# Kernel tuning notes

Hardware: AMD Instinct MI355X
Metric: run time of the kernel (lower is better)

Reference implementation:

```python
import jax, jax.numpy as jnp
import numpy as np

NUM_ZONES = 256  # number of distinct zone ids per image (fill_max of zones)


def setup_inputs() -> dict:
    key = jax.random.key(0)
    k1, k2 = jax.random.split(key)
    B, H, W = 64, 512, 512
    inp = jax.random.normal(k1, (B, 1, H, W), dtype=jnp.float32)
    zones = jax.random.randint(k2, (B, H, W), 0, NUM_ZONES, dtype=jnp.int32)
    return {"input": inp, "zones": zones}


def reference(input, zones):
    # zones branch of CenterExtractor.forward: per-batch scatter_max over zone ids.
    # For each batch element, keep the pixel holding the maximum heatmap value
    # within each zone (segmented argmax), producing a boolean center mask.
    B = input.shape[0]
    x = input.reshape(B, -1)   # [B, N] flattened heatmap
    z = zones.reshape(B, -1)   # [B, N] segment ids

    # per-batch segmented max: [B, NUM_ZONES]
    seg_max = jax.vmap(
        lambda xv, zv: jax.ops.segment_max(xv, zv, num_segments=NUM_ZONES)
    )(x, z)

    # pixel is a center iff it attains its zone's max (ties measure-zero for randn;
    # empty zones have seg_max = -inf and match nothing, mirroring idxs != N filter)
    mask = x == jnp.take_along_axis(seg_max, z, axis=1)  # [B, N] bool

    centermask = mask.reshape(input.shape)  # [B, 1, H, W] bool
    n_centers = jnp.sum(centermask)
    return centermask, n_centers
```

## Files before the change

kernel.cpp:

```cpp
#include <hip/hip_runtime.h>

#define NZ   256
#define NB   64
#define NPIX (512 * 512)

__device__ __forceinline__ unsigned enc(float f) {
    unsigned b = __float_as_uint(f);
    return b ^ ((b & 0x80000000u) ? 0xFFFFFFFFu : 0x80000000u);
}
__device__ __forceinline__ float dec(unsigned u) {
    unsigned b = (u & 0x80000000u) ? (u ^ 0x80000000u) : ~u;
    return __uint_as_float(b);
}

__global__ __launch_bounds__(256) void segmax_kernel(
        const float* __restrict__ inp, const int* __restrict__ zones,
        unsigned* __restrict__ segmax) {
    __shared__ unsigned smax[NZ];
    const int t = threadIdx.x;
    smax[t] = 0u;
    __syncthreads();

    const int blocksPerBatch = NPIX / (256 * 16);
    const int batch = blockIdx.x / blocksPerBatch;
    const int chunk = blockIdx.x % blocksPerBatch;
    const long base = (long)batch * NPIX + (long)chunk * (256 * 16);
    const float4* in4 = (const float4*)(inp + base);
    const int4*   z4  = (const int4*)(zones + base);

#pragma unroll
    for (int it = 0; it < 4; ++it) {
        float4 v = in4[it * 256 + t];
        int4   z = z4[it * 256 + t];
        atomicMax(&smax[z.x], enc(v.x));
        atomicMax(&smax[z.y], enc(v.y));
        atomicMax(&smax[z.z], enc(v.z));
        atomicMax(&smax[z.w], enc(v.w));
    }
    __syncthreads();

    unsigned m = smax[t];
    if (m) atomicMax(&segmax[batch * NZ + t], m);
}

__global__ __launch_bounds__(256) void mask_kernel(
        const float* __restrict__ inp, const int* __restrict__ zones,
        const unsigned* __restrict__ segmax,
        int* __restrict__ mask, int* __restrict__ partial) {
    __shared__ float smax[NZ];
    __shared__ int wsum[4];
    const int t = threadIdx.x;

    const int blocksPerBatch = NPIX / (256 * 16);
    const int batch = blockIdx.x / blocksPerBatch;
    const int chunk = blockIdx.x % blocksPerBatch;

    smax[t] = dec(segmax[batch * NZ + t]);
    __syncthreads();

    const long base = (long)batch * NPIX + (long)chunk * (256 * 16);
    const float4* in4 = (const float4*)(inp + base);
    const int4*   z4  = (const int4*)(zones + base);
    int4* m4 = (int4*)(mask + base);

    int c = 0;
#pragma unroll
    for (int it = 0; it < 4; ++it) {
        float4 v = in4[it * 256 + t];
        int4   z = z4[it * 256 + t];
        int4 m;
        m.x = (v.x == smax[z.x]) ? 1 : 0;
        m.y = (v.y == smax[z.y]) ? 1 : 0;
        m.z = (v.z == smax[z.z]) ? 1 : 0;
        m.w = (v.w == smax[z.w]) ? 1 : 0;
        m4[it * 256 + t] = m;
        c += m.x + m.y + m.z + m.w;
    }

#pragma unroll
    for (int off = 32; off; off >>= 1) c += __shfl_down(c, off);
    if ((t & 63) == 0) wsum[t >> 6] = c;
    __syncthreads();
    if (t == 0) partial[blockIdx.x] = wsum[0] + wsum[1] + wsum[2] + wsum[3];
}

__global__ __launch_bounds__(256) void count_kernel(
        const int* __restrict__ partial, int n, int* __restrict__ count) {
    __shared__ int wsum[4];
    const int t = threadIdx.x;
    int c = 0;
    for (int i = t; i < n; i += 256) c += partial[i];
#pragma unroll
    for (int off = 32; off; off >>= 1) c += __shfl_down(c, off);
    if ((t & 63) == 0) wsum[t >> 6] = c;
    __syncthreads();
    if (t == 0) *count = wsum[0] + wsum[1] + wsum[2] + wsum[3];
}

extern "C" void kernel_launch(void* const* d_in, const int* in_sizes, int n_in,
                              void* d_out, int out_size, void* d_ws, size_t ws_size,
                              hipStream_t stream) {
    const float* inp   = (const float*)d_in[0];
    const int*   zones = (const int*)d_in[1];
    int*         out   = (int*)d_out;
    unsigned*    segmx = (unsigned*)d_ws;
    int*         partial = (int*)((char*)d_ws + NB * NZ * sizeof(unsigned));

    const long nmask = (long)NB * NPIX;
    const int nblocks = NB * (NPIX / 4096);

    hipMemsetAsync(d_ws, 0, (size_t)NB * NZ * sizeof(unsigned), stream);

    segmax_kernel<<<nblocks, 256, 0, stream>>>(inp, zones, segmx);
    mask_kernel<<<nblocks, 256, 0, stream>>>(inp, zones, segmx, out, partial);
    count_kernel<<<1, 256, 0, stream>>>(partial, nblocks, out + nmask);
}
```

Before: 59.23 us.

## Replace global atomics with per-block partial maxima and a separate reduce kernel

The segmented-max stage now writes each block's shared-memory maxima to a partials buffer instead of doing global atomicMax. A new reduce kernel combines the partials per batch and decodes them to floats, which also removes the memset. Each block now processes 32 elements per thread, with all loads batched ahead of the LDS atomics behind a sched_barrier to overlap memory latency. The cost is an extra kernel launch and a round trip of the partials through global memory.

```diff
diff --git a/kernel.cpp b/kernel.cpp
--- a/kernel.cpp
+++ b/kernel.cpp
@@ -1,8 +1,17 @@
 #include <hip/hip_runtime.h>
 
-#define NZ   256
-#define NB   64
-#define NPIX (512 * 512)
+#define NZ    256
+#define NB    64
+#define NPIX  (512 * 512)
+
+#define EPT1  32
+#define CHUNK1 (256 * EPT1)
+#define BPB1  (NPIX / CHUNK1)
+#define NBLK1 (NB * BPB1)
+
+#define CHUNK3 (256 * 16)
+#define BPB3  (NPIX / CHUNK3)
+#define NBLK3 (NB * BPB3)
 
 __device__ __forceinline__ unsigned enc(float f) {
     unsigned b = __float_as_uint(f);
@@ -13,52 +22,69 @@
     return __uint_as_float(b);
 }
 
-__global__ __launch_bounds__(256) void segmax_kernel(
+__global__ __launch_bounds__(256) void segmax_part(
         const float* __restrict__ inp, const int* __restrict__ zones,
-        unsigned* __restrict__ segmax) {
+        unsigned* __restrict__ part) {
     __shared__ unsigned smax[NZ];
     const int t = threadIdx.x;
     smax[t] = 0u;
     __syncthreads();
 
-    const int blocksPerBatch = NPIX / (256 * 16);
-    const int batch = blockIdx.x / blocksPerBatch;
-    const int chunk = blockIdx.x % blocksPerBatch;
-    const long base = (long)batch * NPIX + (long)chunk * (256 * 16);
+    const int batch = blockIdx.x / BPB1;
+    const int chunk = blockIdx.x % BPB1;
+    const long base = (long)batch * NPIX + (long)chunk * CHUNK1;
     const float4* in4 = (const float4*)(inp + base);
     const int4*   z4  = (const int4*)(zones + base);
 
 #pragma unroll
-    for (int it = 0; it < 4; ++it) {
-        float4 v = in4[it * 256 + t];
-        int4   z = z4[it * 256 + t];
-        atomicMax(&smax[z.x], enc(v.x));
-        atomicMax(&smax[z.y], enc(v.y));
-        atomicMax(&smax[z.z], enc(v.z));
-        atomicMax(&smax[z.w], enc(v.w));
+    for (int h = 0; h < EPT1 / 16; ++h) {
+        float4 v[4];
+        int4   z[4];
+#pragma unroll
+        for (int i = 0; i < 4; ++i) {
+            const int idx = (h * 4 + i) * 256 + t;
+            v[i] = in4[idx];
+            z[i] = z4[idx];
+        }
+        __builtin_amdgcn_sched_barrier(0);
+#pragma unroll
+        for (int i = 0; i < 4; ++i) {
+            atomicMax(&smax[z[i].x], enc(v[i].x));
+            atomicMax(&smax[z[i].y], enc(v[i].y));
+            atomicMax(&smax[z[i].z], enc(v[i].z));
+            atomicMax(&smax[z[i].w], enc(v[i].w));
+        }
     }
     __syncthreads();
+    part[(long)blockIdx.x * NZ + t] = smax[t];
+}
 
-    unsigned m = smax[t];
-    if (m) atomicMax(&segmax[batch * NZ + t], m);
+__global__ __launch_bounds__(256) void segmax_reduce(
+        const unsigned* __restrict__ part, float* __restrict__ segf) {
+    const int t = threadIdx.x;
+    const int batch = blockIdx.x;
+    const unsigned* p = part + (long)batch * BPB1 * NZ;
+    unsigned m = 0u;
+#pragma unroll 8
+    for (int c = 0; c < BPB1; ++c) m = max(m, p[c * NZ + t]);
+    segf[batch * NZ + t] = dec(m);
 }
 
 __global__ __launch_bounds__(256) void mask_kernel(
         const float* __restrict__ inp, const int* __restrict__ zones,
-        const unsigned* __restrict__ segmax,
+        const float* __restrict__ segf,
         int* __restrict__ mask, int* __restrict__ partial) {
     __shared__ float smax[NZ];
     __shared__ int wsum[4];
     const int t = threadIdx.x;
 
-    const int blocksPerBatch = NPIX / (256 * 16);
-    const int batch = blockIdx.x / blocksPerBatch;
-    const int chunk = blockIdx.x % blocksPerBatch;
+    const int batch = blockIdx.x / BPB3;
+    const int chunk = blockIdx.x % BPB3;
 
-    smax[t] = dec(segmax[batch * NZ + t]);
+    smax[t] = segf[batch * NZ + t];
     __syncthreads();
 
-    const long base = (long)batch * NPIX + (long)chunk * (256 * 16);
+    const long base = (long)batch * NPIX + (long)chunk * CHUNK3;
     const float4* in4 = (const float4*)(inp + base);
     const int4*   z4  = (const int4*)(zones + base);
     int4* m4 = (int4*)(mask + base);
@@ -103,15 +129,15 @@
     const float* inp   = (const float*)d_in[0];
     const int*   zones = (const int*)d_in[1];
     int*         out   = (int*)d_out;
-    unsigned*    segmx = (unsigned*)d_ws;
-    int*         partial = (int*)((char*)d_ws + NB * NZ * sizeof(unsigned));
+
+    unsigned* part    = (unsigned*)d_ws;
+    float*    segf    = (float*)((char*)d_ws + (size_t)NBLK1 * NZ * 4);
+    int*      partial = (int*)((char*)d_ws + (size_t)NBLK1 * NZ * 4 + (size_t)NB * NZ * 4);
 
     const long nmask = (long)NB * NPIX;
-    const int nblocks = NB * (NPIX / 4096);
 
-    hipMemsetAsync(d_ws, 0, (size_t)NB * NZ * sizeof(unsigned), stream);
-
-    segmax_kernel<<<nblocks, 256, 0, stream>>>(inp, zones, segmx);
-    mask_kernel<<<nblocks, 256, 0, stream>>>(inp, zones, segmx, out, partial);
-    count_kernel<<<1, 256, 0, stream>>>(partial, nblocks, out + nmask);
+    segmax_part  <<<NBLK1, 256, 0, stream>>>(inp, zones, part);
+    segmax_reduce<<<NB,    256, 0, stream>>>(part, segf);
+    mask_kernel  <<<NBLK3, 256, 0, stream>>>(inp, zones, segf, out, partial);
+    count_kernel <<<1,     256, 0, stream>>>(partial, NBLK3, out + nmask);
 }
```

Measured after the change: 56.01 us. 1.06x faster.
